# Kernel optimization log

Measured on AMD Instinct MI355X. Metric: run time of the kernel, lower is better.

The kernel has to match this reference:

```python
import jax, jax.numpy as jnp
import numpy as np

ALPHA = 1.0


def setup_inputs() -> dict:
    key = jax.random.key(0)
    k1, k2 = jax.random.split(key)
    inp = jax.random.normal(k1, (64, 64, 128, 128), dtype=jnp.float32)
    target = jax.random.randint(k2, (64,), 0, 8, dtype=jnp.int64)
    return {"input": inp, "target": target}


def reference(input, target):
    B, C = input.shape[0], input.shape[1]
    x = input.reshape(B, C, -1)                      # [B, C, W]
    W = x.shape[2]
    # Gram matrices, normalized as in computeGram
    G = jnp.einsum('bcw,bdw->bcd', x, x) / (C * W)   # [B, C, C]
    # Pairwise MSE distances D[i,j] = mean((G_i - G_j)^2) over C*C elements
    sq = jnp.sum(G * G, axis=(1, 2))                 # [B]
    dot = jnp.einsum('icd,jcd->ij', G, G)            # [B, B]
    D = (sq[:, None] + sq[None, :] - 2.0 * dot) / (C * C)
    same = target[:, None] == target[None, :]        # [B, B]
    upper = jnp.triu(jnp.ones((B, B), dtype=bool), k=1)
    pos = same & upper                               # positive (i<j) pairs
    neg = ~same                                      # neg[i, a]: target[a] != target[i]
    E = jnp.exp(ALPHA - D)                           # [B, B]
    # Sn[i] = sum over negatives of i of exp(alpha - D(i,k))
    Sn = jnp.sum(jnp.where(neg, E, 0.0), axis=1)     # [B]
    # For a positive pair (i,j), target_i == target_j so neg sets coincide:
    # S[i,j] = Sn[i] + Sn[j]
    S = Sn[:, None] + Sn[None, :]
    J = jnp.log(jnp.where(pos, S, 1.0)) + D          # guard log for masked entries
    P = jnp.sum(pos).astype(jnp.float32)
    loss = jnp.sum(jnp.where(pos, jax.nn.relu(J) ** 2, 0.0)) / (2.0 * P)
    return loss
```

## Files before the change

kernel.cpp:

```cpp
#include <hip/hip_runtime.h>

#define BATCH  64
#define CH     64
#define WFLAT  16384
#define KSPLIT 16
#define KPER   (WFLAT / KSPLIT)
#define BK     128
#define NT     (KPER / BK)
#define LDSS   136

typedef short bf16x8 __attribute__((ext_vector_type(8)));
typedef float f32x4  __attribute__((ext_vector_type(4)));

__device__ __forceinline__ unsigned int f2bf(float f) {
  unsigned int u = __float_as_uint(f);
  return (u + 0x7FFFu + ((u >> 16) & 1u)) >> 16;
}

__global__ __launch_bounds__(256, 4) void gram_kernel(const float* __restrict__ x,
                                                      float* __restrict__ g) {
  const int b  = blockIdx.x & (BATCH - 1);
  const int ks = blockIdx.x >> 6;
  const float* __restrict__ xb = x + (size_t)b * CH * WFLAT + (size_t)ks * KPER;

  __shared__ unsigned short smem[CH * LDSS];

  const int tid  = threadIdx.x;
  const int wave = tid >> 6;
  const int lane = tid & 63;
  const int quad = lane >> 4;
  const int l15  = lane & 15;

  const int trow = tid >> 5;
  const int c4   = tid & 31;
  const float* __restrict__ px = xb + (size_t)trow * WFLAT + c4 * 4;

  f32x4 acc[4];
#pragma unroll
  for (int n = 0; n < 4; n++) acc[n] = (f32x4){0.f, 0.f, 0.f, 0.f};

  float4 stage[8];
#pragma unroll
  for (int r = 0; r < 8; r++)
    stage[r] = *(const float4*)(px + (size_t)r * 8 * WFLAT);

  for (int t = 0; t < NT; t++) {
#pragma unroll
    for (int r = 0; r < 8; r++) {
      const unsigned int lo = f2bf(stage[r].x) | (f2bf(stage[r].y) << 16);
      const unsigned int hi = f2bf(stage[r].z) | (f2bf(stage[r].w) << 16);
      *(uint2*)(&smem[(r * 8 + trow) * LDSS + c4 * 4]) = make_uint2(lo, hi);
    }
    __syncthreads();

    if (t + 1 < NT) {
      const float* __restrict__ pn = px + (size_t)(t + 1) * BK;
#pragma unroll
      for (int r = 0; r < 8; r++)
        stage[r] = *(const float4*)(pn + (size_t)r * 8 * WFLAT);
    }

    const int arow = (wave * 16 + l15) * LDSS;
#pragma unroll
    for (int kk = 0; kk < BK; kk += 32) {
      const int koff = kk + quad * 8;
      const bf16x8 a = *(const bf16x8*)(&smem[arow + koff]);
#pragma unroll
      for (int n = 0; n < 4; n++) {
        const bf16x8 bb = *(const bf16x8*)(&smem[(n * 16 + l15) * LDSS + koff]);
        acc[n] = __builtin_amdgcn_mfma_f32_16x16x32_bf16(a, bb, acc[n], 0, 0, 0);
      }
    }
    __syncthreads();
  }

  const float scale = 1.0f / ((float)CH * (float)WFLAT);
  float* gb = g + (size_t)b * CH * CH;
#pragma unroll
  for (int n = 0; n < 4; n++) {
#pragma unroll
    for (int r = 0; r < 4; r++) {
      const int row = wave * 16 + quad * 4 + r;
      const int col = n * 16 + l15;
      atomicAdd(&gb[row * CH + col], acc[n][r] * scale);
    }
  }
}

__global__ __launch_bounds__(256) void dist_kernel(const float* __restrict__ g,
                                                   float* __restrict__ dpart) {
  const int i  = blockIdx.x & 63;
  const int sl = blockIdx.x >> 6;
  const int tid = threadIdx.x;
  __shared__ float4 gi4[256];

  const float4* gsrc = (const float4*)(g + (size_t)i * (CH * CH)) + sl * 256;
  gi4[tid] = gsrc[tid];
  __syncthreads();

  const int j = tid >> 2;
  const int s = tid & 3;
  const float4* gj = (const float4*)(g + (size_t)j * (CH * CH)) + sl * 256;

  float acc = 0.f;
#pragma unroll 4
  for (int it = 0; it < 64; it++) {
    const int e = it * 4 + s;
    const float4 a  = gi4[e];
    const float4 bv = gj[e];
    const float d0 = a.x - bv.x, d1 = a.y - bv.y;
    const float d2 = a.z - bv.z, d3 = a.w - bv.w;
    acc = fmaf(d0, d0, acc);
    acc = fmaf(d1, d1, acc);
    acc = fmaf(d2, d2, acc);
    acc = fmaf(d3, d3, acc);
  }
  acc += __shfl_xor(acc, 1);
  acc += __shfl_xor(acc, 2);
  if (s == 0) dpart[sl * 4096 + i * 64 + j] = acc * (1.0f / 4096.0f);
}

__global__ __launch_bounds__(64) void loss_kernel(const float* __restrict__ dpart,
                                                  const int* __restrict__ target,
                                                  float* __restrict__ out) {
  __shared__ float dsh[64 * 64];
  __shared__ int   tsh[64];
  __shared__ float snsh[64];
  const int lane = threadIdx.x;

  for (int e = lane; e < 4096; e += 64)
    dsh[e] = dpart[e] + dpart[4096 + e] + dpart[8192 + e] + dpart[12288 + e];
  tsh[lane] = target[lane];
  __syncthreads();

  const int ti = tsh[lane];
  float sn = 0.f;
  for (int k = 0; k < 64; k++) {
    if (tsh[k] != ti) sn += expf(1.0f - dsh[lane * 64 + k]);
  }
  snsh[lane] = sn;
  __syncthreads();

  float lp = 0.f;
  int   pc = 0;
  for (int j = lane + 1; j < 64; j++) {
    if (tsh[j] == ti) {
      const float Jv = logf(sn + snsh[j]) + dsh[lane * 64 + j];
      const float r  = fmaxf(Jv, 0.f);
      lp = fmaf(r, r, lp);
      pc++;
    }
  }
#pragma unroll
  for (int off = 32; off >= 1; off >>= 1) {
    lp += __shfl_down(lp, off);
    pc += __shfl_down(pc, off);
  }
  if (lane == 0) out[0] = lp / (2.0f * (float)pc);
}

extern "C" void kernel_launch(void* const* d_in, const int* in_sizes, int n_in,
                              void* d_out, int out_size, void* d_ws, size_t ws_size,
                              hipStream_t stream) {
  const float* x      = (const float*)d_in[0];
  const int*   target = (const int*)d_in[1];
  float* out = (float*)d_out;

  float* g     = (float*)d_ws;
  float* dpart = g + (size_t)BATCH * CH * CH;

  hipMemsetAsync(g, 0, (size_t)BATCH * CH * CH * sizeof(float), stream);

  gram_kernel<<<BATCH * KSPLIT, 256, 0, stream>>>(x, g);
  dist_kernel<<<BATCH * 4, 256, 0, stream>>>(g, dpart);
  loss_kernel<<<1, 64, 0, stream>>>(dpart, target, out);
}
```

Before: 425.8 us.

## Double-buffer LDS in gram kernel and replace atomics with partial-sum fold

The gram kernel now alternates between two LDS buffers, so only one barrier per K-tile is needed instead of two. Each split-K block writes its partial Gram tile to a dedicated workspace slice instead of using float atomics. A new fold kernel sums the 16 partials per batch and applies the normalisation, which also removes the memset. The cost is double the LDS per block, which may lower occupancy, plus an extra launch and about 4 MB of partial traffic.

```diff
diff --git a/kernel.cpp b/kernel.cpp
--- a/kernel.cpp
+++ b/kernel.cpp
@@ -8,6 +8,7 @@
 #define BK     128
 #define NT     (KPER / BK)
 #define LDSS   136
+#define GSIZE  (CH * CH)
 
 typedef short bf16x8 __attribute__((ext_vector_type(8)));
 typedef float f32x4  __attribute__((ext_vector_type(4)));
@@ -18,12 +19,12 @@
 }
 
 __global__ __launch_bounds__(256, 4) void gram_kernel(const float* __restrict__ x,
-                                                      float* __restrict__ g) {
+                                                      float* __restrict__ gpart) {
   const int b  = blockIdx.x & (BATCH - 1);
   const int ks = blockIdx.x >> 6;
   const float* __restrict__ xb = x + (size_t)b * CH * WFLAT + (size_t)ks * KPER;
 
-  __shared__ unsigned short smem[CH * LDSS];
+  __shared__ unsigned short smem[2][CH * LDSS];
 
   const int tid  = threadIdx.x;
   const int wave = tid >> 6;
@@ -45,13 +46,13 @@
     stage[r] = *(const float4*)(px + (size_t)r * 8 * WFLAT);
 
   for (int t = 0; t < NT; t++) {
+    const int buf = t & 1;
 #pragma unroll
     for (int r = 0; r < 8; r++) {
       const unsigned int lo = f2bf(stage[r].x) | (f2bf(stage[r].y) << 16);
       const unsigned int hi = f2bf(stage[r].z) | (f2bf(stage[r].w) << 16);
-      *(uint2*)(&smem[(r * 8 + trow) * LDSS + c4 * 4]) = make_uint2(lo, hi);
+      *(uint2*)(&smem[buf][(r * 8 + trow) * LDSS + c4 * 4]) = make_uint2(lo, hi);
     }
-    __syncthreads();
 
     if (t + 1 < NT) {
       const float* __restrict__ pn = px + (size_t)(t + 1) * BK;
@@ -60,31 +61,49 @@
         stage[r] = *(const float4*)(pn + (size_t)r * 8 * WFLAT);
     }
 
+    __syncthreads();
+
     const int arow = (wave * 16 + l15) * LDSS;
 #pragma unroll
     for (int kk = 0; kk < BK; kk += 32) {
       const int koff = kk + quad * 8;
-      const bf16x8 a = *(const bf16x8*)(&smem[arow + koff]);
+      const bf16x8 a = *(const bf16x8*)(&smem[buf][arow + koff]);
 #pragma unroll
       for (int n = 0; n < 4; n++) {
-        const bf16x8 bb = *(const bf16x8*)(&smem[(n * 16 + l15) * LDSS + koff]);
+        const bf16x8 bb = *(const bf16x8*)(&smem[buf][(n * 16 + l15) * LDSS + koff]);
         acc[n] = __builtin_amdgcn_mfma_f32_16x16x32_bf16(a, bb, acc[n], 0, 0, 0);
       }
     }
-    __syncthreads();
   }
 
-  const float scale = 1.0f / ((float)CH * (float)WFLAT);
-  float* gb = g + (size_t)b * CH * CH;
+  float* gb = gpart + ((size_t)b * KSPLIT + ks) * GSIZE;
 #pragma unroll
   for (int n = 0; n < 4; n++) {
 #pragma unroll
     for (int r = 0; r < 4; r++) {
       const int row = wave * 16 + quad * 4 + r;
       const int col = n * 16 + l15;
-      atomicAdd(&gb[row * CH + col], acc[n][r] * scale);
+      gb[row * CH + col] = acc[n][r];
     }
   }
+}
+
+__global__ __launch_bounds__(256) void fold_kernel(const float* __restrict__ gpart,
+                                                   float* __restrict__ g) {
+  const int b = blockIdx.x & 63;
+  const int q = blockIdx.x >> 6;
+  const int e = q * 256 + threadIdx.x;
+  const float4* __restrict__ src =
+      (const float4*)(gpart + (size_t)b * KSPLIT * GSIZE) + e;
+  float4 s = make_float4(0.f, 0.f, 0.f, 0.f);
+#pragma unroll
+  for (int ks = 0; ks < KSPLIT; ks++) {
+    const float4 v = src[ks * (GSIZE / 4)];
+    s.x += v.x; s.y += v.y; s.z += v.z; s.w += v.w;
+  }
+  const float scale = 1.0f / ((float)CH * (float)WFLAT);
+  ((float4*)(g + (size_t)b * GSIZE))[e] =
+      make_float4(s.x * scale, s.y * scale, s.z * scale, s.w * scale);
 }
 
 __global__ __launch_bounds__(256) void dist_kernel(const float* __restrict__ g,
@@ -94,13 +113,13 @@
   const int tid = threadIdx.x;
   __shared__ float4 gi4[256];
 
-  const float4* gsrc = (const float4*)(g + (size_t)i * (CH * CH)) + sl * 256;
+  const float4* gsrc = (const float4*)(g + (size_t)i * GSIZE) + sl * 256;
   gi4[tid] = gsrc[tid];
   __syncthreads();
 
   const int j = tid >> 2;
   const int s = tid & 3;
-  const float4* gj = (const float4*)(g + (size_t)j * (CH * CH)) + sl * 256;
+  const float4* gj = (const float4*)(g + (size_t)j * GSIZE) + sl * 256;
 
   float acc = 0.f;
 #pragma unroll 4
@@ -166,12 +185,12 @@
   const int*   target = (const int*)d_in[1];
   float* out = (float*)d_out;
 
-  float* g     = (float*)d_ws;
-  float* dpart = g + (size_t)BATCH * CH * CH;
+  float* gpart = (float*)d_ws;
+  float* g     = gpart + (size_t)BATCH * KSPLIT * GSIZE;
+  float* dpart = g + (size_t)BATCH * GSIZE;
 
-  hipMemsetAsync(g, 0, (size_t)BATCH * CH * CH * sizeof(float), stream);
-
-  gram_kernel<<<BATCH * KSPLIT, 256, 0, stream>>>(x, g);
+  gram_kernel<<<BATCH * KSPLIT, 256, 0, stream>>>(x, gpart);
+  fold_kernel<<<BATCH * 4, 256, 0, stream>>>(gpart, g);
   dist_kernel<<<BATCH * 4, 256, 0, stream>>>(g, dpart);
   loss_kernel<<<1, 64, 0, stream>>>(dpart, target, out);
 }
```

Result: no change. 426.6 us (+0.2%).
